# Optimization experiments

Hardware: AMD Instinct MI355X
Metric: run time of the kernel (lower is better)

The kernel has to match this reference:

```python
import jax, jax.numpy as jnp
import numpy as np

NUM_QUBITS = 16
N_LAYERS = 3
N_PARAMS = 6
BATCH = 64
DIM = 2 ** NUM_QUBITS


def setup_inputs() -> dict:
    key = jax.random.key(0)
    k1, k2, k3, k4, k5 = jax.random.split(key, 5)
    sr = jax.random.normal(k1, (BATCH, DIM), jnp.float32)
    si = jax.random.normal(k2, (BATCH, DIM), jnp.float32)
    nrm = jnp.sqrt(jnp.sum(sr * sr + si * si, axis=1, keepdims=True))
    sr, si = sr / nrm, si / nrm  # StatePrep requires normalized states
    var_params = jax.random.normal(k3, (N_LAYERS, NUM_QUBITS, N_PARAMS), jnp.float32)
    head_w = jax.random.normal(k4, (1, NUM_QUBITS), jnp.float32) / np.sqrt(NUM_QUBITS)
    head_b = jax.random.normal(k5, (1,), jnp.float32) * 0.01
    return {"state_real": sr, "state_imag": si, "var_params": var_params,
            "head_w": head_w, "head_b": head_b}


def _rot_unitary(tx, ty, tz):
    # Fused single-qubit unitary U = RZ(tz) @ RY(ty) @ RX(tx)
    cx, sx = jnp.cos(tx / 2), jnp.sin(tx / 2)
    cy, sy = jnp.cos(ty / 2), jnp.sin(ty / 2)
    Rx = jnp.stack([jnp.stack([cx + 0j, -1j * sx]),
                    jnp.stack([-1j * sx, cx + 0j])])
    Ry = jnp.stack([jnp.stack([cy + 0j, -sy + 0j]),
                    jnp.stack([sy + 0j, cy + 0j])])
    ez = jnp.exp(-1j * tz / 2)
    zero = jnp.zeros_like(ez)
    Rz = jnp.stack([jnp.stack([ez, zero]), jnp.stack([zero, jnp.conj(ez)])])
    return (Rz @ Ry @ Rx).astype(jnp.complex64)


def _circuit_features(state_real, state_imag, var_params):
    psi = jax.lax.complex(state_real, state_imag)  # (B, 2^n), wire 0 = MSB
    B = psi.shape[0]
    for l in range(N_LAYERS):
        for q in range(NUM_QUBITS):
            U = _rot_unitary(var_params[l, q, 0], var_params[l, q, 1], var_params[l, q, 2])
            psi = psi.reshape(B, 2 ** q, 2, -1)  # isolate wire q
            psi = jnp.einsum('ij,bljr->blir', U, psi)
        for q in range(NUM_QUBITS - 1):
            # CNOT(control=q, target=q+1): flip target axis where control=1
            psi = psi.reshape(B, 2 ** q, 2, 2, -1)
            psi = jnp.concatenate([psi[:, :, 0:1], psi[:, :, 1:2, ::-1]], axis=2)
        psi = psi.reshape(B, -1)
    probs = psi.real ** 2 + psi.imag ** 2  # (B, 2^n)
    feats = []
    for q in range(NUM_QUBITS):
        p = probs.reshape(B, 2 ** q, 2, -1)
        feats.append(p[:, :, 0, :].sum(axis=(1, 2)) - p[:, :, 1, :].sum(axis=(1, 2)))
    return jnp.stack(feats, axis=1)  # (B, n) expvals of PauliZ


def reference(state_real, state_imag, var_params, head_w, head_b):
    feats = _circuit_features(state_real, state_imag, var_params)
    return (feats @ head_w.T + head_b)[:, 0]  # (B,)
```

## Files before the change

kernel.cpp:

```cpp
#include <hip/hip_runtime.h>


typedef float f2 __attribute__((ext_vector_type(2)));
typedef unsigned int u2 __attribute__((ext_vector_type(2)));

struct G8 { float r00,i00,r01,i01,r10,i10,r11,i11; };

__device__ __forceinline__ f2 mkf2(float a, float b) { f2 r; r.x = a; r.y = b; return r; }
__device__ __forceinline__ f2 swp(f2 v) { f2 r; r.x = v.y; r.y = v.x; return r; }
__device__ __forceinline__ f2 sn(f2 v) { f2 r; r.x = -v.y; r.y = v.x; return r; }

__device__ __forceinline__ float px32s(float v, bool lo) {
  u2 r = __builtin_amdgcn_permlane32_swap(__float_as_uint(v), __float_as_uint(v), false, false);
  return __uint_as_float(lo ? r.y : r.x);
}
__device__ __forceinline__ f2 px32(f2 v, bool lo) { return mkf2(px32s(v.x,lo), px32s(v.y,lo)); }
template<int CTRL>
__device__ __forceinline__ float dpps(float v) {
  return __int_as_float(__builtin_amdgcn_mov_dpp(__float_as_int(v), CTRL, 0xF, 0xF, false));
}
__device__ __forceinline__ f2 ex2(f2 v, int mask, bool lo) {
  if (mask == 32) return px32(v, lo);
  if (mask == 1)  return mkf2(dpps<0xB1>(v.x), dpps<0xB1>(v.y));
  if (mask == 2)  return mkf2(dpps<0x4E>(v.x), dpps<0x4E>(v.y));
  if (mask == 3)  return mkf2(dpps<0x1B>(v.x), dpps<0x1B>(v.y));
  return mkf2(__shfl_xor(v.x, mask), __shfl_xor(v.y, mask));
}

__device__ __forceinline__ G8 loadG(const float* p) {
  G8 g;
  g.r00=p[0]; g.i00=p[1]; g.r01=p[2]; g.i01=p[3];
  g.r10=p[4]; g.i10=p[5]; g.r11=p[6]; g.i11=p[7];
  return g;
}

struct CP { f2 dr, di, br, bi; };
__device__ __forceinline__ CP mkCP(const G8& g, int w) {
  CP c;
  const float a = w ? g.r11 : g.r00, b = w ? g.i11 : g.i00;
  const float p = w ? g.r10 : g.r01, q = w ? g.i10 : g.i01;
  c.dr = mkf2(a,a); c.di = mkf2(b,b); c.br = mkf2(p,p); c.bi = mkf2(q,q);
  return c;
}
__device__ __forceinline__ void supdP(const CP& c, f2& x, f2 p) {
  x = __builtin_elementwise_fma(c.dr, x,
       __builtin_elementwise_fma(c.di, sn(x),
        __builtin_elementwise_fma(c.br, p, c.bi * sn(p))));
}

struct C2 { f2 dr, di, br, bi; };
__device__ __forceinline__ C2 mkC2(const G8& g, int wlo, int whi) {
  C2 c;
  c.dr = mkf2(wlo ? g.r11 : g.r00, whi ? g.r11 : g.r00);
  c.di = mkf2(wlo ? g.i11 : g.i00, whi ? g.i11 : g.i00);
  c.br = mkf2(wlo ? g.r10 : g.r01, whi ? g.r10 : g.r01);
  c.bi = mkf2(wlo ? g.i10 : g.i01, whi ? g.i10 : g.i01);
  return c;
}
__device__ __forceinline__ void supd2(const C2& c, f2& xr, f2& xi, f2 pr, f2 pi) {
  f2 nr = __builtin_elementwise_fma(c.dr, xr,
           __builtin_elementwise_fma(c.di, -xi,
            __builtin_elementwise_fma(c.br, pr, c.bi * (-pi))));
  f2 ni = __builtin_elementwise_fma(c.dr, xi,
           __builtin_elementwise_fma(c.di, xr,
            __builtin_elementwise_fma(c.br, pi, c.bi * pr)));
  xr = nr; xi = ni;
}

__device__ __forceinline__ void buildU(const float* __restrict__ vp, float* U) {
  const int i = threadIdx.x;
  if (i < 48) {
    const float tx = vp[i*6+0], ty = vp[i*6+1], tz = vp[i*6+2];
    float sx, cx, sy, cy, sz, cz;
    sincosf(0.5f*tx, &sx, &cx);
    sincosf(0.5f*ty, &sy, &cy);
    sincosf(0.5f*tz, &sz, &cz);
    const float m00r = cy*cx,  m00i = sy*sx;
    const float m01r = -sy*cx, m01i = -cy*sx;
    const float m10r = sy*cx,  m10i = -cy*sx;
    const float m11r = cy*cx,  m11i = -sy*sx;
    float* o = U + i*8;
    o[0] = cz*m00r + sz*m00i;  o[1] = cz*m00i - sz*m00r;
    o[2] = cz*m01r + sz*m01i;  o[3] = cz*m01i - sz*m01r;
    o[4] = cz*m10r - sz*m10i;  o[5] = cz*m10i + sz*m10r;
    o[6] = cz*m11r - sz*m11i;  o[7] = cz*m11i + sz*m11r;
  }
}

#define GU(l, w) loadG(Ush + ((l)*16 + (w))*8)

__global__ void __launch_bounds__(256, 2)
kA(const float* __restrict__ sr, const float* __restrict__ si,
   float* __restrict__ dr, float* __restrict__ di,
   const float* __restrict__ vp, const float* __restrict__ hb, float* __restrict__ out) {
  __shared__ float Ush[384];
  buildU(vp, Ush);
  const int t = threadIdx.x;
  const int l = t & 63, wv = t >> 6;
  const int l5 = (l >> 5) & 1, l4 = (l >> 4) & 1;
  const bool lo32 = (l & 32) == 0;
  const int b = blockIdx.x >> 3, c = blockIdx.x & 7;
  if (blockIdx.x == 0 && t < 64) out[t] = hb[0];
  __syncthreads();

  const size_t bb = (size_t)b << 16;
  const int tb = (l5 << 10) | (l4 << 9) | (c << 6) | (wv << 4) | (l & 15);
  f2 x[32];
  #pragma unroll
  for (int k = 0; k < 32; ++k) {
    const size_t a = bb + (k << 11) + tb;
    x[k] = mkf2(sr[a], si[a]);
  }

#define RPA(CA, CB, A, B) { f2 tt = x[A]; supdP(CA, x[A], x[B]); supdP(CB, x[B], tt); }

  #pragma unroll
  for (int g = 0; g < 5; ++g) {
    const int kb = 4 - g;
    const G8 U = GU(0, g);
    const CP c0 = mkCP(U, 0), c1 = mkCP(U, 1);
    #pragma unroll
    for (int p = 0; p < 16; ++p) {
      const int i0 = ((p >> kb) << (kb + 1)) | (p & ((1 << kb) - 1));
      RPA(c0, c1, i0, i0 | (1 << kb));
    }
  }
  { const G8 U = GU(0,5); const CP cc = mkCP(U, l5);
    #pragma unroll
    for (int a = 0; a < 32; ++a) supdP(cc, x[a], ex2(x[a], 32, lo32)); }
  { const G8 U = GU(0,6); const CP cc = mkCP(U, l4);
    #pragma unroll
    for (int a = 0; a < 32; ++a) supdP(cc, x[a], ex2(x[a], 16, lo32)); }
  { const G8 U = GU(1,0); const CP c0 = mkCP(U,0), c1 = mkCP(U,1);
    #pragma unroll
    for (int k = 0; k < 32; ++k) if (!((k>>4)&1)) RPA(c0, c1, k, k^24); }
  { const G8 U = GU(1,1); const CP c0 = mkCP(U,0), c1 = mkCP(U,1);
    #pragma unroll
    for (int k = 0; k < 32; ++k) if (!((k>>3)&1)) {
      const int f = (k>>4)&1;
      RPA(f?c1:c0, f?c0:c1, k, k^12);
    } }
  { const G8 U = GU(1,2); const CP c0 = mkCP(U,0), c1 = mkCP(U,1);
    #pragma unroll
    for (int k = 0; k < 32; ++k) if (!((k>>2)&1)) {
      const int f = ((k>>4)^(k>>3))&1;
      RPA(f?c1:c0, f?c0:c1, k, k^6);
    } }
  { const G8 U = GU(1,3); const CP c0 = mkCP(U,0), c1 = mkCP(U,1);
    #pragma unroll
    for (int k = 0; k < 32; ++k) if (!((k>>1)&1)) {
      const int f = ((k>>4)^(k>>3)^(k>>2))&1;
      RPA(f?c1:c0, f?c0:c1, k, k^3);
    } }
  { const G8 U = GU(1,4); const CP c0 = mkCP(U,0), c1 = mkCP(U,1);
    #pragma unroll
    for (int m = 0; m < 16; ++m) {
      const int k0 = 2*m, k1 = 2*m+1;
      f2 p0 = ex2(x[k1], 32, lo32), p1 = ex2(x[k0], 32, lo32);
      const int w0 = __builtin_popcount(k0)&1;
      supdP(w0?c1:c0, x[k0], p0);
      supdP(w0?c0:c1, x[k1], p1);
    } }
  { const G8 U = GU(1,5); const CP cA = mkCP(U, l5), cB = mkCP(U, l5^1);
    #pragma unroll
    for (int k = 0; k < 32; ++k) {
      f2 p = ex2(x[k], 48, lo32);
      supdP((__builtin_popcount(k)&1)?cB:cA, x[k], p);
    } }
  { const G8 U = GU(2,0); const CP c0 = mkCP(U,0), c1 = mkCP(U,1);
    #pragma unroll
    for (int k = 0; k < 32; ++k) if (!((k>>4)&1)) RPA(c0, c1, k, k^20); }
  { const G8 U = GU(2,1); const CP c0 = mkCP(U,0), c1 = mkCP(U,1);
    #pragma unroll
    for (int k = 0; k < 32; ++k) if (!((k>>3)&1)) RPA(c0, c1, k, k^10); }
  { const G8 U = GU(2,2); const CP c0 = mkCP(U,0), c1 = mkCP(U,1);
    #pragma unroll
    for (int k = 0; k < 32; ++k) if (!((k>>2)&1)) {
      const int f = (k>>4)&1;
      RPA(f?c1:c0, f?c0:c1, k, k^5);
    } }
  { const G8 U = GU(2,3); const CP c0 = mkCP(U,0), c1 = mkCP(U,1);
    #pragma unroll
    for (int k = 0; k < 32; ++k) if (!((k>>1)&1)) {
      f2 p0 = ex2(x[k^2], 32, lo32), p1 = ex2(x[k], 32, lo32);
      const int f = (k>>3)&1;
      supdP(f?c1:c0, x[k], p0);
      supdP(f?c0:c1, x[k^2], p1);
    } }

  #pragma unroll
  for (int k = 0; k < 32; ++k) {
    const size_t a = bb + (k << 11) + tb;
    dr[a] = x[k].x; di[a] = x[k].y;
  }
#undef RPA
}

__device__ __forceinline__ int SA2(int i) { return i ^ (((i >> 5) & 7) << 1); }

__global__ void __launch_bounds__(256, 4)
kB(const float* __restrict__ sr, const float* __restrict__ si,
   const float* __restrict__ vp, const float* __restrict__ hw, float* __restrict__ out) {
  __shared__ float lds[8192];
  __shared__ float Ush[384];
  __shared__ float red[4];
  buildU(vp, Ush);
  const int t = threadIdx.x;
  const int l = t & 63, wv = t >> 6;
  const bool lo32 = (l & 32) == 0;
  const int b = blockIdx.x >> 4, h4 = blockIdx.x & 15;
  __syncthreads();

  const int ph4 = __builtin_popcount(h4) & 1;
  const int pA4 = ((h4 >> 1) ^ (h4 >> 3)) & 1;
  const int pB4 = (h4 ^ (h4 >> 2)) & 1;
  const size_t base0 = ((size_t)b << 16) | (h4 << 12) | (wv << 8) | (l << 2);

  f2 xr2[8], xi2[8];
  #pragma unroll
  for (int kk = 0; kk < 2; ++kk) {
    const float4 r0 = *(const float4*)(sr + base0 + (kk << 10));
    const float4 r1 = *(const float4*)(sr + base0 + (kk << 10) + 2048);
    const float4 i0 = *(const float4*)(si + base0 + (kk << 10));
    const float4 i1 = *(const float4*)(si + base0 + (kk << 10) + 2048);
    xr2[kk*4+0] = mkf2(r0.x, r1.x); xr2[kk*4+1] = mkf2(r0.y, r1.y);
    xr2[kk*4+2] = mkf2(r0.z, r1.z); xr2[kk*4+3] = mkf2(r0.w, r1.w);
    xi2[kk*4+0] = mkf2(i0.x, i1.x); xi2[kk*4+1] = mkf2(i0.y, i1.y);
    xi2[kk*4+2] = mkf2(i0.z, i1.z); xi2[kk*4+3] = mkf2(i0.w, i1.w);
  }

#define RP2(CA, CB, A, B) { f2 tr = xr2[A], ti = xi2[A]; \
    supd2(CA, xr2[A], xi2[A], xr2[B], xi2[B]); \
    supd2(CB, xr2[B], xi2[B], tr, ti); }

  #pragma unroll
  for (int g = 0; g < 6; ++g) {
    const int mask = 32 >> g;
    const G8 U = GU(0, 8 + g);
    const int hi = (l >> (5 - g)) & 1;
    const C2 cc = mkC2(U, hi, hi);
    #pragma unroll
    for (int s = 0; s < 8; ++s) {
      f2 pr = ex2(xr2[s], mask, lo32), pi = ex2(xi2[s], mask, lo32);
      supd2(cc, xr2[s], xi2[s], pr, pi);
    }
  }
  { const G8 U = GU(0,14);
    const C2 c0 = mkC2(U,0,0), c1 = mkC2(U,1,1);
    #pragma unroll
    for (int kk = 0; kk < 2; ++kk)
      #pragma unroll
      for (int e0 = 0; e0 < 2; ++e0) RP2(c0, c1, kk*4+e0, kk*4+e0+2); }
  { const G8 U = GU(0,15);
    const C2 c0 = mkC2(U,0,0), c1 = mkC2(U,1,1);
    #pragma unroll
    for (int kk = 0; kk < 2; ++kk) {
      RP2(c0, c1, kk*4+0, kk*4+1);
      RP2(c0, c1, kk*4+2, kk*4+3);
    } }

  #pragma unroll
  for (int kk = 0; kk < 2; ++kk)
    #pragma unroll
    for (int e = 0; e < 4; ++e) {
      const int fi = ((kk << 10) | (wv << 8) | (l << 2) | e) << 1;
      *(f2*)&lds[SA2(fi)] = xr2[kk*4+e];
      *(f2*)&lds[4096 + SA2(fi)] = xi2[kk*4+e];
    }
  __syncthreads();
  #pragma unroll
  for (int s3 = 0; s3 < 8; ++s3) {
    const int fi = ((s3 << 8) | (l << 2) | wv) << 1;
    xr2[s3] = *(f2*)&lds[SA2(fi)];
    xi2[s3] = *(f2*)&lds[4096 + SA2(fi)];
  }

  const int l5=(l>>5)&1, l4=(l>>4)&1, l3=(l>>3)&1, l2=(l>>2)&1, l1=(l>>1)&1, l0=l&1;
  { const G8 U = GU(0,7);
    const C2 c0 = mkC2(U,0,0), c1 = mkC2(U,1,1);
    #pragma unroll
    for (int s3 = 0; s3 < 8; s3 += 2) RP2(c0, c1, s3, s3^1); }
  { const G8 U = GU(1,6);
    const C2 cA = mkC2(U, ph4, ph4^1), cB = mkC2(U, ph4^1, ph4);
    #pragma unroll
    for (int s3 = 0; s3 < 8; ++s3) if (!((s3>>1)&1)) {
      const int f = (s3>>2)&1;
      RP2(f?cB:cA, f?cA:cB, s3, s3^3);
    } }
  { const G8 U = GU(1,7);
    const C2 cA = mkC2(U, ph4, ph4^1), cB = mkC2(U, ph4^1, ph4);
    #pragma unroll
    for (int s3 = 0; s3 < 8; s3 += 2) {
      f2 p0r = ex2(xr2[s3^1], 32, lo32), p0i = ex2(xi2[s3^1], 32, lo32);
      f2 p1r = ex2(xr2[s3],   32, lo32), p1i = ex2(xi2[s3],   32, lo32);
      const int f = ((s3>>2)^(s3>>1))&1;
      supd2(f?cB:cA, xr2[s3], xi2[s3], p0r, p0i);
      supd2(f?cA:cB, xr2[s3^1], xi2[s3^1], p1r, p1i);
    } }
  #pragma unroll
  for (int g = 0; g < 5; ++g) {
    const int mask = 48 >> g;
    const G8 U = GU(1, 8 + g);
    const int lp = (g==0)? l5 : (g==1)? (l4^l5) : (g==2)? (l3^l4^l5)
                 : (g==3)? (l2^l3^l4^l5) : (l1^l2^l3^l4^l5);
    const C2 cA = mkC2(U, (lp^ph4)&1, (lp^ph4^1)&1);
    const C2 cB = mkC2(U, (lp^ph4^1)&1, (lp^ph4)&1);
    #pragma unroll
    for (int s3 = 0; s3 < 8; ++s3) {
      f2 pr = ex2(xr2[s3], mask, lo32), pi = ex2(xi2[s3], mask, lo32);
      supd2((__builtin_popcount(s3)&1)?cB:cA, xr2[s3], xi2[s3], pr, pi);
    }
  }
  { const G8 U = GU(2,4);
    const C2 cc = mkC2(U, pA4, pA4^1);
    #pragma unroll
    for (int s3 = 0; s3 < 8; ++s3) if (!((s3>>1)&1)) {
      f2 tr = xr2[s3], ti = xi2[s3];
      supd2(cc, xr2[s3], xi2[s3], swp(xr2[s3^2]), swp(xi2[s3^2]));
      supd2(cc, xr2[s3^2], xi2[s3^2], swp(tr), swp(ti));
    } }
  { const G8 U = GU(2,5);
    const C2 cA = mkC2(U, pB4, pB4), cB = mkC2(U, pB4^1, pB4^1);
    #pragma unroll
    for (int s3 = 0; s3 < 4; ++s3) RP2(cA, cB, s3, s3^5); }
  { const G8 U = GU(2,6);
    const C2 cA = mkC2(U, pA4, pA4^1), cB = mkC2(U, pA4^1, pA4);
    #pragma unroll
    for (int s3 = 0; s3 < 8; ++s3) if (!((s3>>1)&1)) {
      f2 p0r = ex2(xr2[s3^2], 32, lo32), p0i = ex2(xi2[s3^2], 32, lo32);
      f2 p1r = ex2(xr2[s3],   32, lo32), p1i = ex2(xi2[s3],   32, lo32);
      supd2(cA, xr2[s3], xi2[s3], p0r, p0i);
      supd2(cB, xr2[s3^2], xi2[s3^2], p1r, p1i);
    } }
  { const G8 U = GU(2,7);
    const C2 cA = mkC2(U, pB4, pB4), cB = mkC2(U, pB4^1, pB4^1);
    #pragma unroll
    for (int s3 = 0; s3 < 8; s3 += 2) {
      f2 p0r = ex2(xr2[s3^1], 16, lo32), p0i = ex2(xi2[s3^1], 16, lo32);
      f2 p1r = ex2(xr2[s3],   16, lo32), p1i = ex2(xi2[s3],   16, lo32);
      const int f = (s3>>2)&1;
      supd2(f?cB:cA, xr2[s3], xi2[s3], p0r, p0i);
      supd2(f?cA:cB, xr2[s3^1], xi2[s3^1], p1r, p1i);
    } }
  #pragma unroll
  for (int g = 0; g < 3; ++g) {
    const int mask = (g == 0) ? 40 : (g == 1) ? 20 : 10;
    const G8 U = GU(2, 8 + g);
    int mpar, blo, bhi;
    if      (g == 0) { mpar = 2; blo = (l5^pA4)&1;      bhi = blo^1; }
    else if (g == 1) { mpar = 5; blo = (l4^pB4)&1;      bhi = blo;   }
    else             { mpar = 2; blo = (l3^l5^pA4)&1;   bhi = blo^1; }
    const C2 cA = mkC2(U, blo, bhi), cB = mkC2(U, blo^1, bhi^1);
    #pragma unroll
    for (int s3 = 0; s3 < 8; ++s3) {
      f2 pr = ex2(xr2[s3], mask, lo32), pi = ex2(xi2[s3], mask, lo32);
      supd2((__builtin_popcount(s3 & mpar)&1)?cB:cA, xr2[s3], xi2[s3], pr, pi);
    }
  }

  __syncthreads();
  #pragma unroll
  for (int s3 = 0; s3 < 8; ++s3) {
    const int fi = ((s3 << 8) | (l << 2) | wv) << 1;
    *(f2*)&lds[SA2(fi)] = xr2[s3];
    *(f2*)&lds[4096 + SA2(fi)] = xi2[s3];
  }
  __syncthreads();
  #pragma unroll
  for (int kk = 0; kk < 2; ++kk)
    #pragma unroll
    for (int e = 0; e < 4; ++e) {
      const int fi = ((kk << 10) | (wv << 8) | (l << 2) | e) << 1;
      xr2[kk*4+e] = *(f2*)&lds[SA2(fi)];
      xi2[kk*4+e] = *(f2*)&lds[4096 + SA2(fi)];
    }

  const int wv1 = (wv >> 1) & 1, wv0 = wv & 1;
  const int RPlo  = (__builtin_popcount(l) ^ __builtin_popcount(wv) ^ ph4) & 1;
  const int oddTl = (l1 ^ l3 ^ l5 ^ wv1 ^ pA4) & 1;
  const int evB   = (l0 ^ l2 ^ l4 ^ wv0 ^ pB4) & 1;
  { const G8 U = GU(1,13);
    const C2 cA = mkC2(U, RPlo, RPlo^1), cB = mkC2(U, RPlo^1, RPlo);
    #pragma unroll
    for (int kk = 0; kk < 2; ++kk) {
      const C2& cc = kk ? cB : cA;
      #pragma unroll
      for (int e0 = 0; e0 < 2; ++e0) {
        const int a = kk*4 + e0, a2 = a + 2;
        f2 par = ex2(xr2[a2], 1, lo32), pai = ex2(xi2[a2], 1, lo32);
        f2 pbr = ex2(xr2[a],  1, lo32), pbi = ex2(xi2[a],  1, lo32);
        supd2(cc, xr2[a],  xi2[a],  par, pai);
        supd2(cc, xr2[a2], xi2[a2], pbr, pbi);
      }
    } }
  { const G8 U = GU(1,14);
    const C2 cA = mkC2(U, RPlo, RPlo^1), cB = mkC2(U, RPlo^1, RPlo);
    #pragma unroll
    for (int kk = 0; kk < 2; ++kk) {
      RP2(kk?cB:cA, kk?cA:cB, kk*4+0, kk*4+3);
      RP2(kk?cB:cA, kk?cA:cB, kk*4+1, kk*4+2);
    } }
  { const G8 U = GU(1,15);
    const C2 cA = mkC2(U, RPlo, RPlo^1), cB = mkC2(U, RPlo^1, RPlo);
    #pragma unroll
    for (int kk = 0; kk < 2; ++kk) {
      RP2(kk?cB:cA, kk?cA:cB, kk*4+0, kk*4+1);
      RP2(kk?cA:cB, kk?cB:cA, kk*4+2, kk*4+3);
    } }
  { const G8 U = GU(2,11);
    const int b4 = (l2 ^ l4 ^ wv0 ^ pB4) & 1;
    const C2 cA = mkC2(U, b4, b4), cB = mkC2(U, b4^1, b4^1);
    #pragma unroll
    for (int s = 0; s < 8; ++s) {
      f2 pr = ex2(xr2[s], 5, lo32), pi = ex2(xi2[s], 5, lo32);
      supd2((s>>2)?cB:cA, xr2[s], xi2[s], pr, pi);
    } }
  { const G8 U = GU(2,12);
    const C2 cc = mkC2(U, oddTl, oddTl^1);
    #pragma unroll
    for (int kk = 0; kk < 2; ++kk)
      #pragma unroll
      for (int e0 = 0; e0 < 2; ++e0) {
        const int a = kk*4 + e0, a2 = a + 2;
        f2 par = ex2(xr2[a2], 2, lo32), pai = ex2(xi2[a2], 2, lo32);
        f2 pbr = ex2(xr2[a],  2, lo32), pbi = ex2(xi2[a],  2, lo32);
        supd2(cc, xr2[a],  xi2[a],  par, pai);
        supd2(cc, xr2[a2], xi2[a2], pbr, pbi);
      } }
  { const G8 U = GU(2,13);
    const C2 cA = mkC2(U, evB, evB), cB = mkC2(U, evB^1, evB^1);
    #pragma unroll
    for (int kk = 0; kk < 2; ++kk) {
      const C2& cc = kk ? cB : cA;
      #pragma unroll
      for (int e0 = 0; e0 < 4; e0 += 2) {
        const int a = kk*4 + e0, a2 = a + 1;
        f2 par = ex2(xr2[a2], 1, lo32), pai = ex2(xi2[a2], 1, lo32);
        f2 pbr = ex2(xr2[a],  1, lo32), pbi = ex2(xi2[a],  1, lo32);
        supd2(cc, xr2[a],  xi2[a],  par, pai);
        supd2(cc, xr2[a2], xi2[a2], pbr, pbi);
      }
    } }
  { const G8 U = GU(2,14);
    const C2 cA = mkC2(U, oddTl, oddTl^1), cB = mkC2(U, oddTl^1, oddTl);
    #pragma unroll
    for (int kk = 0; kk < 2; ++kk) {
      RP2(cA, cB, kk*4+0, kk*4+2);
      RP2(cA, cB, kk*4+1, kk*4+3);
    } }
  { const G8 U = GU(2,15);
    const C2 cA = mkC2(U, evB, evB), cB = mkC2(U, evB^1, evB^1);
    #pragma unroll
    for (int kk = 0; kk < 2; ++kk) {
      RP2(kk?cB:cA, kk?cA:cB, kk*4+0, kk*4+1);
      RP2(kk?cB:cA, kk?cA:cB, kk*4+2, kk*4+3);
    } }

  #pragma unroll
  for (int s = 0; s < 8; ++s)
    xr2[s] = xr2[s]*xr2[s] + xi2[s]*xi2[s];
  const int jloc = (h4 << 12) | (wv << 8) | (l << 2);
  float hsum = 0.f;
  #pragma unroll
  for (int q = 0; q < 16; ++q) {
    const int M = (0x3333 << (15 - q)) & 0xFFFF;
    f2 acc = mkf2(0.f, 0.f);
    #pragma unroll
    for (int s = 0; s < 8; ++s) {
      const int amp = ((s >> 2) << 10) | (s & 3);
      if (__builtin_popcount(amp & M) & 1) acc -= xr2[s]; else acc += xr2[s];
    }
    float sv = acc.x + (((M >> 11) & 1) ? -acc.y : acc.y);
    if (__builtin_popcount(jloc & M) & 1) sv = -sv;
    hsum += hw[q] * sv;
  }
  #pragma unroll
  for (int o = 32; o >= 1; o >>= 1) hsum += __shfl_xor(hsum, o);
  if ((t & 63) == 0) red[wv] = hsum;
  __syncthreads();
  if (t == 0) atomicAdd(out + b, red[0] + red[1] + red[2] + red[3]);
#undef RP2
}

extern "C" void kernel_launch(void* const* d_in, const int* in_sizes, int n_in,
                              void* d_out, int out_size, void* d_ws, size_t ws_size,
                              hipStream_t stream) {
  const float* in_r = (const float*)d_in[0];
  const float* in_i = (const float*)d_in[1];
  const float* vp = (const float*)d_in[2];
  const float* hw = (const float*)d_in[3];
  const float* hb = (const float*)d_in[4];
  float* out = (float*)d_out;

  float* ws_r = (float*)d_ws;
  float* ws_i = ws_r + 4194304ull;

  kA<<<512,  256, 0, stream>>>(in_r, in_i, ws_r, ws_i, vp, hb, out);
  kB<<<1024, 256, 0, stream>>>(ws_r, ws_i, vp, hw, out);
}
```

Measured before the change: 137.2 us.

## Halve per-thread state in kA and use permlane16 swaps for lane exchanges

kA now holds 16 amplitudes per thread instead of 32. Three qubits are mapped to lane bits instead of two, and twice as many blocks are launched with a higher occupancy bound. This lowers register pressure so more waves can run at once and hide global memory latency. The cost is more cross-lane exchanges, so ex2 gains permlane16_swap paths for lane masks 16, 48 and 40 in place of generic shuffles. The gate-to-register index mapping in kA is rewritten to match.

```diff
diff --git a/kernel.cpp b/kernel.cpp
--- a/kernel.cpp
+++ b/kernel.cpp
@@ -15,12 +15,28 @@
   return __uint_as_float(lo ? r.y : r.x);
 }
 __device__ __forceinline__ f2 px32(f2 v, bool lo) { return mkf2(px32s(v.x,lo), px32s(v.y,lo)); }
+#if __has_builtin(__builtin_amdgcn_permlane16_swap)
+__device__ __forceinline__ float px16s(float v, bool lo16) {
+  u2 r = __builtin_amdgcn_permlane16_swap(__float_as_uint(v), __float_as_uint(v), false, false);
+  return __uint_as_float(lo16 ? r.y : r.x);
+}
+#else
+__device__ __forceinline__ float px16s(float v, bool lo16) {
+  return __int_as_float(__builtin_amdgcn_ds_swizzle(__float_as_int(v), 0x401F));
+}
+#endif
+__device__ __forceinline__ f2 px16(f2 v, bool lo) { return mkf2(px16s(v.x,lo), px16s(v.y,lo)); }
 template<int CTRL>
 __device__ __forceinline__ float dpps(float v) {
   return __int_as_float(__builtin_amdgcn_mov_dpp(__float_as_int(v), CTRL, 0xF, 0xF, false));
 }
-__device__ __forceinline__ f2 ex2(f2 v, int mask, bool lo) {
-  if (mask == 32) return px32(v, lo);
+__device__ __forceinline__ f2 ex2(f2 v, int mask, int l) {
+  const bool lo32 = (l & 32) == 0, lo16 = (l & 16) == 0;
+  if (mask == 32) return px32(v, lo32);
+  if (mask == 16) return px16(v, lo16);
+  if (mask == 48) return px16(px32(v, lo32), lo16);
+  if (mask == 40) { f2 w = px32(v, lo32);
+                    return mkf2(__shfl_xor(w.x, 8), __shfl_xor(w.y, 8)); }
   if (mask == 1)  return mkf2(dpps<0xB1>(v.x), dpps<0xB1>(v.y));
   if (mask == 2)  return mkf2(dpps<0x4E>(v.x), dpps<0x4E>(v.y));
   if (mask == 3)  return mkf2(dpps<0x1B>(v.x), dpps<0x1B>(v.y));
@@ -89,7 +105,7 @@
 
 #define GU(l, w) loadG(Ush + ((l)*16 + (w))*8)
 
-__global__ void __launch_bounds__(256, 2)
+__global__ void __launch_bounds__(256, 4)
 kA(const float* __restrict__ sr, const float* __restrict__ si,
    float* __restrict__ dr, float* __restrict__ di,
    const float* __restrict__ vp, const float* __restrict__ hb, float* __restrict__ out) {
@@ -97,100 +113,105 @@
   buildU(vp, Ush);
   const int t = threadIdx.x;
   const int l = t & 63, wv = t >> 6;
-  const int l5 = (l >> 5) & 1, l4 = (l >> 4) & 1;
-  const bool lo32 = (l & 32) == 0;
-  const int b = blockIdx.x >> 3, c = blockIdx.x & 7;
+  const int L5 = (l >> 5) & 1, L4 = (l >> 4) & 1, L3 = (l >> 3) & 1;
+  const int b = blockIdx.x >> 4, g4 = blockIdx.x & 15;
   if (blockIdx.x == 0 && t < 64) out[t] = hb[0];
   __syncthreads();
 
   const size_t bb = (size_t)b << 16;
-  const int tb = (l5 << 10) | (l4 << 9) | (c << 6) | (wv << 4) | (l & 15);
-  f2 x[32];
-  #pragma unroll
-  for (int k = 0; k < 32; ++k) {
-    const size_t a = bb + (k << 11) + tb;
+  const int tb = (L5 << 11) | (L4 << 10) | (L3 << 9) | (g4 << 5) | (wv << 3) | (l & 7);
+  f2 x[16];
+  #pragma unroll
+  for (int k = 0; k < 16; ++k) {
+    const size_t a = bb + (k << 12) + tb;
     x[k] = mkf2(sr[a], si[a]);
   }
 
 #define RPA(CA, CB, A, B) { f2 tt = x[A]; supdP(CA, x[A], x[B]); supdP(CB, x[B], tt); }
 
   #pragma unroll
-  for (int g = 0; g < 5; ++g) {
-    const int kb = 4 - g;
+  for (int g = 0; g < 4; ++g) {
+    const int kb = 3 - g;
     const G8 U = GU(0, g);
     const CP c0 = mkCP(U, 0), c1 = mkCP(U, 1);
     #pragma unroll
-    for (int p = 0; p < 16; ++p) {
+    for (int p = 0; p < 8; ++p) {
       const int i0 = ((p >> kb) << (kb + 1)) | (p & ((1 << kb) - 1));
       RPA(c0, c1, i0, i0 | (1 << kb));
     }
   }
-  { const G8 U = GU(0,5); const CP cc = mkCP(U, l5);
-    #pragma unroll
-    for (int a = 0; a < 32; ++a) supdP(cc, x[a], ex2(x[a], 32, lo32)); }
-  { const G8 U = GU(0,6); const CP cc = mkCP(U, l4);
-    #pragma unroll
-    for (int a = 0; a < 32; ++a) supdP(cc, x[a], ex2(x[a], 16, lo32)); }
+  { const G8 U = GU(0,4); const CP cc = mkCP(U, L5);
+    #pragma unroll
+    for (int a = 0; a < 16; ++a) supdP(cc, x[a], ex2(x[a], 32, l)); }
+  { const G8 U = GU(0,5); const CP cc = mkCP(U, L4);
+    #pragma unroll
+    for (int a = 0; a < 16; ++a) supdP(cc, x[a], ex2(x[a], 16, l)); }
+  { const G8 U = GU(0,6); const CP cc = mkCP(U, L3);
+    #pragma unroll
+    for (int a = 0; a < 16; ++a) supdP(cc, x[a], ex2(x[a], 8, l)); }
   { const G8 U = GU(1,0); const CP c0 = mkCP(U,0), c1 = mkCP(U,1);
     #pragma unroll
-    for (int k = 0; k < 32; ++k) if (!((k>>4)&1)) RPA(c0, c1, k, k^24); }
+    for (int k = 0; k < 16; ++k) if (!((k>>3)&1)) RPA(c0, c1, k, k^12); }
   { const G8 U = GU(1,1); const CP c0 = mkCP(U,0), c1 = mkCP(U,1);
     #pragma unroll
-    for (int k = 0; k < 32; ++k) if (!((k>>3)&1)) {
-      const int f = (k>>4)&1;
-      RPA(f?c1:c0, f?c0:c1, k, k^12);
+    for (int k = 0; k < 16; ++k) if (!((k>>2)&1)) {
+      const int f = (k>>3)&1;
+      RPA(f?c1:c0, f?c0:c1, k, k^6);
     } }
   { const G8 U = GU(1,2); const CP c0 = mkCP(U,0), c1 = mkCP(U,1);
     #pragma unroll
-    for (int k = 0; k < 32; ++k) if (!((k>>2)&1)) {
-      const int f = ((k>>4)^(k>>3))&1;
-      RPA(f?c1:c0, f?c0:c1, k, k^6);
+    for (int k = 0; k < 16; ++k) if (!((k>>1)&1)) {
+      const int f = ((k>>3)^(k>>2))&1;
+      RPA(f?c1:c0, f?c0:c1, k, k^3);
     } }
   { const G8 U = GU(1,3); const CP c0 = mkCP(U,0), c1 = mkCP(U,1);
     #pragma unroll
-    for (int k = 0; k < 32; ++k) if (!((k>>1)&1)) {
-      const int f = ((k>>4)^(k>>3)^(k>>2))&1;
-      RPA(f?c1:c0, f?c0:c1, k, k^3);
-    } }
-  { const G8 U = GU(1,4); const CP c0 = mkCP(U,0), c1 = mkCP(U,1);
-    #pragma unroll
-    for (int m = 0; m < 16; ++m) {
+    for (int m = 0; m < 8; ++m) {
       const int k0 = 2*m, k1 = 2*m+1;
-      f2 p0 = ex2(x[k1], 32, lo32), p1 = ex2(x[k0], 32, lo32);
+      f2 p0 = ex2(x[k1], 32, l), p1 = ex2(x[k0], 32, l);
       const int w0 = __builtin_popcount(k0)&1;
       supdP(w0?c1:c0, x[k0], p0);
       supdP(w0?c0:c1, x[k1], p1);
     } }
-  { const G8 U = GU(1,5); const CP cA = mkCP(U, l5), cB = mkCP(U, l5^1);
-    #pragma unroll
-    for (int k = 0; k < 32; ++k) {
-      f2 p = ex2(x[k], 48, lo32);
+  { const G8 U = GU(1,4); const CP cA = mkCP(U, L5), cB = mkCP(U, L5^1);
+    #pragma unroll
+    for (int k = 0; k < 16; ++k) {
+      f2 p = ex2(x[k], 48, l);
       supdP((__builtin_popcount(k)&1)?cB:cA, x[k], p);
     } }
+  { const G8 U = GU(1,5); const int v = (L5^L4)&1;
+    const CP cA = mkCP(U, v), cB = mkCP(U, v^1);
+    #pragma unroll
+    for (int k = 0; k < 16; ++k) {
+      f2 p = ex2(x[k], 24, l);
+      supdP((__builtin_popcount(k)&1)?cB:cA, x[k], p);
+    } }
   { const G8 U = GU(2,0); const CP c0 = mkCP(U,0), c1 = mkCP(U,1);
     #pragma unroll
-    for (int k = 0; k < 32; ++k) if (!((k>>4)&1)) RPA(c0, c1, k, k^20); }
+    for (int k = 0; k < 16; ++k) if (!((k>>3)&1)) RPA(c0, c1, k, k^10); }
   { const G8 U = GU(2,1); const CP c0 = mkCP(U,0), c1 = mkCP(U,1);
     #pragma unroll
-    for (int k = 0; k < 32; ++k) if (!((k>>3)&1)) RPA(c0, c1, k, k^10); }
+    for (int k = 0; k < 16; ++k) if (!((k>>2)&1)) RPA(c0, c1, k, k^5); }
   { const G8 U = GU(2,2); const CP c0 = mkCP(U,0), c1 = mkCP(U,1);
     #pragma unroll
-    for (int k = 0; k < 32; ++k) if (!((k>>2)&1)) {
-      const int f = (k>>4)&1;
-      RPA(f?c1:c0, f?c0:c1, k, k^5);
-    } }
-  { const G8 U = GU(2,3); const CP c0 = mkCP(U,0), c1 = mkCP(U,1);
-    #pragma unroll
-    for (int k = 0; k < 32; ++k) if (!((k>>1)&1)) {
-      f2 p0 = ex2(x[k^2], 32, lo32), p1 = ex2(x[k], 32, lo32);
+    for (int k = 0; k < 16; ++k) if (!((k>>1)&1)) {
+      f2 p0 = ex2(x[k^2], 32, l), p1 = ex2(x[k], 32, l);
       const int f = (k>>3)&1;
       supdP(f?c1:c0, x[k], p0);
       supdP(f?c0:c1, x[k^2], p1);
     } }
-
-  #pragma unroll
-  for (int k = 0; k < 32; ++k) {
-    const size_t a = bb + (k << 11) + tb;
+  { const G8 U = GU(2,3); const CP c0 = mkCP(U,0), c1 = mkCP(U,1);
+    #pragma unroll
+    for (int k = 0; k < 16; k += 2) {
+      f2 p0 = ex2(x[k^1], 16, l), p1 = ex2(x[k], 16, l);
+      const int f = (k>>2)&1;
+      supdP(f?c1:c0, x[k], p0);
+      supdP(f?c0:c1, x[k^1], p1);
+    } }
+
+  #pragma unroll
+  for (int k = 0; k < 16; ++k) {
+    const size_t a = bb + (k << 12) + tb;
     dr[a] = x[k].x; di[a] = x[k].y;
   }
 #undef RPA
@@ -207,7 +228,6 @@
   buildU(vp, Ush);
   const int t = threadIdx.x;
   const int l = t & 63, wv = t >> 6;
-  const bool lo32 = (l & 32) == 0;
   const int b = blockIdx.x >> 4, h4 = blockIdx.x & 15;
   __syncthreads();
 
@@ -241,7 +261,7 @@
     const C2 cc = mkC2(U, hi, hi);
     #pragma unroll
     for (int s = 0; s < 8; ++s) {
-      f2 pr = ex2(xr2[s], mask, lo32), pi = ex2(xi2[s], mask, lo32);
+      f2 pr = ex2(xr2[s], mask, l), pi = ex2(xi2[s], mask, l);
       supd2(cc, xr2[s], xi2[s], pr, pi);
     }
   }
@@ -291,8 +311,8 @@
     const C2 cA = mkC2(U, ph4, ph4^1), cB = mkC2(U, ph4^1, ph4);
     #pragma unroll
     for (int s3 = 0; s3 < 8; s3 += 2) {
-      f2 p0r = ex2(xr2[s3^1], 32, lo32), p0i = ex2(xi2[s3^1], 32, lo32);
-      f2 p1r = ex2(xr2[s3],   32, lo32), p1i = ex2(xi2[s3],   32, lo32);
+      f2 p0r = ex2(xr2[s3^1], 32, l), p0i = ex2(xi2[s3^1], 32, l);
+      f2 p1r = ex2(xr2[s3],   32, l), p1i = ex2(xi2[s3],   32, l);
       const int f = ((s3>>2)^(s3>>1))&1;
       supd2(f?cB:cA, xr2[s3], xi2[s3], p0r, p0i);
       supd2(f?cA:cB, xr2[s3^1], xi2[s3^1], p1r, p1i);
@@ -307,7 +327,7 @@
     const C2 cB = mkC2(U, (lp^ph4^1)&1, (lp^ph4)&1);
     #pragma unroll
     for (int s3 = 0; s3 < 8; ++s3) {
-      f2 pr = ex2(xr2[s3], mask, lo32), pi = ex2(xi2[s3], mask, lo32);
+      f2 pr = ex2(xr2[s3], mask, l), pi = ex2(xi2[s3], mask, l);
       supd2((__builtin_popcount(s3)&1)?cB:cA, xr2[s3], xi2[s3], pr, pi);
     }
   }
@@ -327,8 +347,8 @@
     const C2 cA = mkC2(U, pA4, pA4^1), cB = mkC2(U, pA4^1, pA4);
     #pragma unroll
     for (int s3 = 0; s3 < 8; ++s3) if (!((s3>>1)&1)) {
-      f2 p0r = ex2(xr2[s3^2], 32, lo32), p0i = ex2(xi2[s3^2], 32, lo32);
-      f2 p1r = ex2(xr2[s3],   32, lo32), p1i = ex2(xi2[s3],   32, lo32);
+      f2 p0r = ex2(xr2[s3^2], 32, l), p0i = ex2(xi2[s3^2], 32, l);
+      f2 p1r = ex2(xr2[s3],   32, l), p1i = ex2(xi2[s3],   32, l);
       supd2(cA, xr2[s3], xi2[s3], p0r, p0i);
       supd2(cB, xr2[s3^2], xi2[s3^2], p1r, p1i);
     } }
@@ -336,8 +356,8 @@
     const C2 cA = mkC2(U, pB4, pB4), cB = mkC2(U, pB4^1, pB4^1);
     #pragma unroll
     for (int s3 = 0; s3 < 8; s3 += 2) {
-      f2 p0r = ex2(xr2[s3^1], 16, lo32), p0i = ex2(xi2[s3^1], 16, lo32);
-      f2 p1r = ex2(xr2[s3],   16, lo32), p1i = ex2(xi2[s3],   16, lo32);
+      f2 p0r = ex2(xr2[s3^1], 16, l), p0i = ex2(xi2[s3^1], 16, l);
+      f2 p1r = ex2(xr2[s3],   16, l), p1i = ex2(xi2[s3],   16, l);
       const int f = (s3>>2)&1;
       supd2(f?cB:cA, xr2[s3], xi2[s3], p0r, p0i);
       supd2(f?cA:cB, xr2[s3^1], xi2[s3^1], p1r, p1i);
@@ -353,7 +373,7 @@
     const C2 cA = mkC2(U, blo, bhi), cB = mkC2(U, blo^1, bhi^1);
     #pragma unroll
     for (int s3 = 0; s3 < 8; ++s3) {
-      f2 pr = ex2(xr2[s3], mask, lo32), pi = ex2(xi2[s3], mask, lo32);
+      f2 pr = ex2(xr2[s3], mask, l), pi = ex2(xi2[s3], mask, l);
       supd2((__builtin_popcount(s3 & mpar)&1)?cB:cA, xr2[s3], xi2[s3], pr, pi);
     }
   }
@@ -387,8 +407,8 @@
       #pragma unroll
       for (int e0 = 0; e0 < 2; ++e0) {
         const int a = kk*4 + e0, a2 = a + 2;
-        f2 par = ex2(xr2[a2], 1, lo32), pai = ex2(xi2[a2], 1, lo32);
-        f2 pbr = ex2(xr2[a],  1, lo32), pbi = ex2(xi2[a],  1, lo32);
+        f2 par = ex2(xr2[a2], 1, l), pai = ex2(xi2[a2], 1, l);
+        f2 pbr = ex2(xr2[a],  1, l), pbi = ex2(xi2[a],  1, l);
         supd2(cc, xr2[a],  xi2[a],  par, pai);
         supd2(cc, xr2[a2], xi2[a2], pbr, pbi);
       }
@@ -412,7 +432,7 @@
     const C2 cA = mkC2(U, b4, b4), cB = mkC2(U, b4^1, b4^1);
     #pragma unroll
     for (int s = 0; s < 8; ++s) {
-      f2 pr = ex2(xr2[s], 5, lo32), pi = ex2(xi2[s], 5, lo32);
+      f2 pr = ex2(xr2[s], 5, l), pi = ex2(xi2[s], 5, l);
       supd2((s>>2)?cB:cA, xr2[s], xi2[s], pr, pi);
     } }
   { const G8 U = GU(2,12);
@@ -422,8 +442,8 @@
       #pragma unroll
       for (int e0 = 0; e0 < 2; ++e0) {
         const int a = kk*4 + e0, a2 = a + 2;
-        f2 par = ex2(xr2[a2], 2, lo32), pai = ex2(xi2[a2], 2, lo32);
-        f2 pbr = ex2(xr2[a],  2, lo32), pbi = ex2(xi2[a],  2, lo32);
+        f2 par = ex2(xr2[a2], 2, l), pai = ex2(xi2[a2], 2, l);
+        f2 pbr = ex2(xr2[a],  2, l), pbi = ex2(xi2[a],  2, l);
         supd2(cc, xr2[a],  xi2[a],  par, pai);
         supd2(cc, xr2[a2], xi2[a2], pbr, pbi);
       } }
@@ -435,8 +455,8 @@
       #pragma unroll
       for (int e0 = 0; e0 < 4; e0 += 2) {
         const int a = kk*4 + e0, a2 = a + 1;
-        f2 par = ex2(xr2[a2], 1, lo32), pai = ex2(xi2[a2], 1, lo32);
-        f2 pbr = ex2(xr2[a],  1, lo32), pbi = ex2(xi2[a],  1, lo32);
+        f2 par = ex2(xr2[a2], 1, l), pai = ex2(xi2[a2], 1, l);
+        f2 pbr = ex2(xr2[a],  1, l), pbi = ex2(xi2[a],  1, l);
         supd2(cc, xr2[a],  xi2[a],  par, pai);
         supd2(cc, xr2[a2], xi2[a2], pbr, pbi);
       }
@@ -495,6 +515,6 @@
   float* ws_r = (float*)d_ws;
   float* ws_i = ws_r + 4194304ull;
 
-  kA<<<512,  256, 0, stream>>>(in_r, in_i, ws_r, ws_i, vp, hb, out);
+  kA<<<1024, 256, 0, stream>>>(in_r, in_i, ws_r, ws_i, vp, hb, out);
   kB<<<1024, 256, 0, stream>>>(ws_r, ws_i, vp, hw, out);
 }
```

Result: slower. 146.3 us (+6.7%).
